# Kernel tuning notes

Measured on AMD Instinct MI355X. Metric: run time of the kernel, lower is better.

## Reference

```python
import jax, jax.numpy as jnp
import numpy as np

B = 8192          # batch_size = len(embedds)
D = 512           # ll_p['num_channels'][-1]
C = 100           # n_classes
N_LAB = 4096      # int(B * plb), plb = 0.5
MAX_ITER = 30     # gtg_i
TOL = 1e-3        # gtg_t
ENT_EPS = 1e-20


def _mlp(x, W1, b1, W2, b2, W3, b3, Wc, bc):
    h = jax.nn.relu(x @ W1 + b1)
    h = jax.nn.relu(h @ W2 + b2)
    h = jax.nn.relu(h @ W3 + b3)
    return (h @ Wc + bc)[:, 0]  # squeeze -> [B]


def _entropy(X):
    # per-row Shannon entropy (bits), as in ALGTG utils
    return -jnp.sum(X * jnp.log2(X + ENT_EPS), axis=1)


def _gtg_entropy_hist(embedds, labels):
    # get_A: cos_sim -> zero diagonal -> clamp [0,1] -> 'mean' threshold -> 'diversity' (1-A)
    n = jnp.maximum(jnp.linalg.norm(embedds, axis=-1, keepdims=True), 1e-12)
    E = embedds / n
    A = E @ E.T                                   # [B,B]
    A = A * (1.0 - jnp.eye(B, dtype=A.dtype))     # fill_diagonal_(0)
    A = jnp.clip(A, 0.0, 1.0)
    A = jnp.where(A < jnp.mean(A), 0.0, A)        # AM_threshold_strategy == 'mean'
    A = 1.0 - A                                   # AM_strategy == 'diversity'

    # get_X: labeled rows one-hot, unlabeled rows uniform 1/C
    lab = jnp.arange(B) < N_LAB
    X0 = jnp.where(lab[:, None],
                   jax.nn.one_hot(labels, C, dtype=jnp.float32),
                   jnp.full((B, C), 1.0 / C, jnp.float32))
    hist0 = jnp.zeros((B, MAX_ITER), jnp.float32)
    unlab = ~lab

    def cond(s):
        _X, _h, i, err = s
        return (err > TOL) & (i < MAX_ITER)

    def body(s):
        X, hist, i, _err = s
        Xn = X * (A @ X)                          # replicator dynamics step
        Xn = Xn / jnp.sum(Xn, axis=1, keepdims=True)
        ent = _entropy(Xn)
        hist = hist.at[:, i].set(jnp.where(unlab, ent, 0.0))
        return (Xn, hist, i + 1, jnp.linalg.norm(Xn - X))

    init = (X0, hist0, jnp.array(0, jnp.int32), jnp.array(jnp.inf, jnp.float32))
    _, hist, _, _ = jax.lax.while_loop(cond, body, init)
    return hist


def setup_inputs() -> dict:
    key = jax.random.key(0)
    ks = jax.random.split(key, 11)
    d2, d4, d8 = D // 2, D // 4, D // 8

    def lin(k, fi, fo):
        return jax.random.normal(k, (fi, fo), jnp.float32) / np.float32(np.sqrt(fi))

    return {
        'features': jax.random.normal(ks[0], (B, 64), jnp.float32),
        'embedds': jax.random.normal(ks[1], (B, D), jnp.float32),
        'labels': jax.random.randint(ks[2], (B,), 0, C),
        'W1': lin(ks[3], D, d2), 'b1': jnp.zeros((d2,), jnp.float32),
        'W2': lin(ks[4], d2, d4), 'b2': jnp.zeros((d4,), jnp.float32),
        'W3': lin(ks[5], d4, d8), 'b3': jnp.zeros((d8,), jnp.float32),
        'Wc': lin(ks[6], d8, 1), 'bc': jnp.zeros((1,), jnp.float32),
    }


def reference(features, embedds, labels, W1, b1, W2, b2, W3, b3, Wc, bc):
    y_pred = _mlp(embedds, W1, b1, W2, b2, W3, b3, Wc, bc)        # [B]
    hist = _gtg_entropy_hist(embedds, labels)                      # [B, MAX_ITER]
    y_true = jnp.mean(hist, axis=1)                                # ent_strategy == 'mean'
    labeled_mask = jnp.arange(B) < N_LAB                           # bool [B]
    return (y_pred, y_true, labeled_mask)
```

## Files before the change

### kernel.cpp

```cpp
#include <hip/hip_runtime.h>
#include <hip/hip_bf16.h>
#include <math.h>

namespace {
constexpr int BROWS = 8192;
constexpr int NLAB  = 4096;
constexpr int NUNL  = 4096;
constexpr int CREAL = 100;
constexpr int CPAD  = 112;
constexpr int DIM   = 512;
constexpr int MAXIT = 30;

constexpr size_t MiB = 1ull << 20;
constexpr size_t OFF_S    = 0;
constexpr size_t OFF_AU   = 64 * MiB;
constexpr size_t OFF_EB   = 96 * MiB;
constexpr size_t OFF_XT0  = 96 * MiB;
constexpr size_t OFF_XT1  = 98 * MiB;
constexpr size_t OFF_XU   = 100 * MiB;
constexpr size_t OFF_PL   = 102 * MiB;
constexpr size_t OFF_HIST = 104 * MiB;
constexpr size_t OFF_ERR  = 104 * MiB + 16384;
constexpr size_t OFF_MS   = 104 * MiB + 16768;
constexpr size_t OFF_RN   = 104 * MiB + 32768;
constexpr size_t MEMSET_LEN = 20480;
}

typedef __attribute__((ext_vector_type(8))) short short8;
typedef __attribute__((ext_vector_type(4))) float floatx4;

__device__ inline ushort f2bf(float f) {
  __hip_bfloat16 h = __float2bfloat16(f);
  union { __hip_bfloat16 b; ushort u; } c; c.b = h; return c.u;
}
__device__ inline float bf2f(ushort u) {
  union { ushort u; __hip_bfloat16 b; } c; c.u = u;
  return __bfloat162float(c.b);
}

__global__ __launch_bounds__(64) void k_prep(const float* __restrict__ emb,
                                             ushort* __restrict__ Eb,
                                             float* __restrict__ rn) {
  int row = blockIdx.x, l = threadIdx.x;
  const float4* e4 = (const float4*)(emb + (size_t)row * DIM);
  float4 a = e4[2 * l], b = e4[2 * l + 1];
  float f[8] = {a.x, a.y, a.z, a.w, b.x, b.y, b.z, b.w};
  float s = 0.f;
#pragma unroll
  for (int q = 0; q < 8; q++) s += f[q] * f[q];
#pragma unroll
  for (int m = 1; m < 64; m <<= 1) s += __shfl_xor(s, m);
  if (l == 0) rn[row] = 1.0f / fmaxf(sqrtf(s), 1e-12f);
  union { short8 v; ushort u[8]; } o;
#pragma unroll
  for (int q = 0; q < 8; q++) o.u[q] = f2bf(f[q]);
  *(short8*)(Eb + (size_t)row * DIM + l * 8) = o.v;
}

__global__ __launch_bounds__(256) void k_initX(ushort* __restrict__ X0,
                                               ushort* __restrict__ X1,
                                               float* __restrict__ Xu,
                                               const int* __restrict__ labels) {
  int j = blockIdx.x * 256 + threadIdx.x;
  int c = blockIdx.y;
  float v;
  if (j < NLAB) v = (labels[j] == c) ? 1.0f : 0.0f;
  else          v = (c < CREAL) ? 0.01f : 0.0f;
  ushort b = f2bf(v);
  X0[(size_t)c * BROWS + j] = b;
  X1[(size_t)c * BROWS + j] = b;
  if (j >= NLAB) Xu[(size_t)(j - NLAB) * CPAD + c] = (c < CREAL) ? 0.01f : 0.0f;
}

__global__ __launch_bounds__(256) void k_mlp(const float* __restrict__ emb,
                                             const float* __restrict__ W1, const float* __restrict__ b1,
                                             const float* __restrict__ W2, const float* __restrict__ b2,
                                             const float* __restrict__ W3, const float* __restrict__ b3,
                                             const float* __restrict__ Wc, const float* __restrict__ bc,
                                             float* __restrict__ out) {
  __shared__ float xs[4][512];
  __shared__ float h1[4][256];
  __shared__ float h2[4][128];
  __shared__ float h3[4][64];
  int t = threadIdx.x;
  int r0 = blockIdx.x * 4;
  {
    const float4* src = (const float4*)(emb + (size_t)r0 * DIM);
    float4* dst = (float4*)&xs[0][0];
    dst[t] = src[t];
    dst[t + 256] = src[t + 256];
  }
  __syncthreads();
  {
    float a0 = 0.f, a1 = 0.f, a2 = 0.f, a3 = 0.f;
    for (int k = 0; k < 512; k++) {
      float w = W1[k * 256 + t];
      a0 = fmaf(xs[0][k], w, a0);
      a1 = fmaf(xs[1][k], w, a1);
      a2 = fmaf(xs[2][k], w, a2);
      a3 = fmaf(xs[3][k], w, a3);
    }
    float bb = b1[t];
    h1[0][t] = fmaxf(a0 + bb, 0.f);
    h1[1][t] = fmaxf(a1 + bb, 0.f);
    h1[2][t] = fmaxf(a2 + bb, 0.f);
    h1[3][t] = fmaxf(a3 + bb, 0.f);
  }
  __syncthreads();
  {
    int c = t & 127, rb = (t >> 7) * 2;
    float a0 = 0.f, a1 = 0.f;
    for (int k = 0; k < 256; k++) {
      float w = W2[k * 128 + c];
      a0 = fmaf(h1[rb][k], w, a0);
      a1 = fmaf(h1[rb + 1][k], w, a1);
    }
    float bb = b2[c];
    h2[rb][c] = fmaxf(a0 + bb, 0.f);
    h2[rb + 1][c] = fmaxf(a1 + bb, 0.f);
  }
  __syncthreads();
  {
    int c = t & 63, r = t >> 6;
    float a = 0.f;
    for (int k = 0; k < 128; k++) a = fmaf(h2[r][k], W3[k * 64 + c], a);
    h3[r][c] = fmaxf(a + b3[c], 0.f);
  }
  __syncthreads();
  {
    int r = t >> 6, l = t & 63;
    float v = h3[r][l] * Wc[l];
#pragma unroll
    for (int m = 32; m; m >>= 1) v += __shfl_down(v, m);
    if (l == 0) out[r0 + r] = v + bc[0];
  }
}

__global__ __launch_bounds__(256) void k_simM(const ushort* __restrict__ Eb,
                                              const float* __restrict__ rn,
                                              ushort* __restrict__ S,
                                              double* __restrict__ meansum) {
  int x = blockIdx.x, y = blockIdx.y;
  if (x < 32 && y > x) return;
  __shared__ ushort Ei[128 * 40];
  __shared__ ushort Ej[128 * 40];
  __shared__ float redbuf[4];

  int t = threadIdx.x;
  int w = t >> 6, lane = t & 63;
  int m = lane & 15, g = lane >> 4;
  int ib = (w >> 1) * 64, jb = (w & 1) * 64;
  int i0 = x * 128, j0 = y * 128;

  floatx4 acc[4][4];
#pragma unroll
  for (int a = 0; a < 4; a++)
#pragma unroll
    for (int b = 0; b < 4; b++) acc[a][b] = (floatx4)0.0f;

  int lrow = t >> 1, lhalf = (t & 1) * 16;
  for (int kt = 0; kt < DIM; kt += 32) {
    __syncthreads();
    {
      const ushort* gi = Eb + (size_t)(i0 + lrow) * DIM + kt + lhalf;
      const ushort* gj = Eb + (size_t)(j0 + lrow) * DIM + kt + lhalf;
      int o = lrow * 40 + lhalf;
      *(short8*)&Ei[o]     = *(const short8*)gi;
      *(short8*)&Ei[o + 8] = *(const short8*)(gi + 8);
      *(short8*)&Ej[o]     = *(const short8*)gj;
      *(short8*)&Ej[o + 8] = *(const short8*)(gj + 8);
    }
    __syncthreads();

    short8 ah[4], bh[4];
#pragma unroll
    for (int rt = 0; rt < 4; rt++) ah[rt] = *(const short8*)&Ei[(ib + rt * 16 + m) * 40 + g * 8];
#pragma unroll
    for (int ct = 0; ct < 4; ct++) bh[ct] = *(const short8*)&Ej[(jb + ct * 16 + m) * 40 + g * 8];
#pragma unroll
    for (int rt = 0; rt < 4; rt++)
#pragma unroll
      for (int ct = 0; ct < 4; ct++)
        acc[rt][ct] = __builtin_amdgcn_mfma_f32_16x16x32_bf16(ah[rt], bh[ct], acc[rt][ct], 0, 0, 0);
  }

  bool dostore = (x >= 32);
  bool isdiag  = (x == y);
  float weight = (x < 32) ? (isdiag ? 1.0f : 2.0f) : ((y < 32) ? 2.0f : 1.0f);
  float lsum = 0.f;
#pragma unroll
  for (int rt = 0; rt < 4; rt++) {
    int gi0 = i0 + ib + rt * 16 + g * 4;
    float4 rni = *(const float4*)(rn + gi0);
#pragma unroll
    for (int ct = 0; ct < 4; ct++) {
      int gj = j0 + jb + ct * 16 + m;
      float rnj = rn[gj];
#pragma unroll
      for (int r = 0; r < 4; r++) {
        int gi = gi0 + r;
        float rv = (r == 0) ? rni.x : (r == 1) ? rni.y : (r == 2) ? rni.z : rni.w;
        float s = acc[rt][ct][r] * rv * rnj;
        if (isdiag && gi == gj) s = 0.f;
        s = fminf(fmaxf(s, 0.f), 1.f);
        lsum += s;
        if (dostore) S[(size_t)(gi - NLAB) * BROWS + gj] = f2bf(s);
      }
    }
  }
  lsum *= weight;
#pragma unroll
  for (int d = 1; d < 64; d <<= 1) lsum += __shfl_xor(lsum, d);
  if (lane == 0) redbuf[w] = lsum;
  __syncthreads();
  if (t == 0) atomicAdd(meansum, (double)(redbuf[0] + redbuf[1] + redbuf[2] + redbuf[3]));
}

__global__ __launch_bounds__(1024, 4) void k_iter(const ushort* __restrict__ S,
                                                  ushort* __restrict__ Au,
                                                  const ushort* __restrict__ XTr,
                                                  ushort* __restrict__ XTw,
                                                  float* __restrict__ Xu,
                                                  float* __restrict__ Plab,
                                                  float* __restrict__ hist,
                                                  float* __restrict__ errsq,
                                                  const double* __restrict__ ms,
                                                  int it) {
  if (it > 0 && errsq[it - 1] <= 1e-6f) return;
  __shared__ float part[8][16 * 113];
  __shared__ float Pbuf[16 * 114];
  __shared__ float dsqbuf[16];
  ushort* xbuf = (ushort*)&part[0][0];
  int t = threadIdx.x;
  int w = t >> 6, lane = t & 63;
  int m = lane & 15, g = lane >> 4;
  int r0 = blockIdx.x * 16;

  float2 xo = make_float2(0.f, 0.f);
  if (lane < 56) xo = *(const float2*)(Xu + (size_t)(r0 + w) * CPAD + lane * 2);
  float pl_pre[2] = {0.f, 0.f};
  if (it > 0) {
#pragma unroll
    for (int q = 0; q < 2; q++) {
      int idx = t + q * 1024;
      if (idx < 16 * CPAD)
        pl_pre[q] = Plab[(size_t)(r0 + idx / CPAD) * CPAD + idx % CPAD];
    }
  }

  floatx4 acc[7];
#pragma unroll
  for (int c = 0; c < 7; c++) acc[c] = (floatx4)0.0f;

  if (it == 0) {
    float mean = (float)(ms[0] * (1.0 / ((double)BROWS * (double)BROWS)));
    int kw = w * 512;
    for (int ks = 0; ks < 16; ks++) {
      int kk = kw + ks * 32;
      size_t so = (size_t)(r0 + m) * BROWS + kk + g * 8;
      short8 a = *(const short8*)(S + so);
      union { short8 v; ushort u[8]; } ua; ua.v = a;
#pragma unroll
      for (int e = 0; e < 8; e++) {
        float s = bf2f(ua.u[e]);
        float av = (s < mean) ? 1.0f : 1.0f - s;
        ua.u[e] = f2bf(av);
      }
      a = ua.v;
      if (w >= 8)
        *(short8*)(Au + (size_t)(r0 + m) * NUNL + (kk - NLAB) + g * 8) = a;
#pragma unroll
      for (int ct = 0; ct < 7; ct++) {
        short8 b = *(const short8*)(XTr + (size_t)(ct * 16 + m) * BROWS + kk + g * 8);
        acc[ct] = __builtin_amdgcn_mfma_f32_16x16x32_bf16(a, b, acc[ct], 0, 0, 0);
      }
    }
  } else {
    int kw = w * 256;
    size_t abase = (size_t)(r0 + m) * NUNL + kw + g * 8;
    size_t bbase = (size_t)m * BROWS + NLAB + kw + g * 8;
    for (int ks = 0; ks < 8; ks++) {
      short8 a = *(const short8*)(Au + abase + ks * 32);
#pragma unroll
      for (int ct = 0; ct < 7; ct++) {
        short8 b = *(const short8*)(XTr + bbase + (size_t)ct * 16 * BROWS + ks * 32);
        acc[ct] = __builtin_amdgcn_mfma_f32_16x16x32_bf16(a, b, acc[ct], 0, 0, 0);
      }
    }
  }

  if (w < 8) {
#pragma unroll
    for (int ct = 0; ct < 7; ct++)
#pragma unroll
      for (int r = 0; r < 4; r++)
        part[w][(g * 4 + r) * 113 + ct * 16 + m] = acc[ct][r];
  }
  __syncthreads();
  float sA[2] = {0.f, 0.f}, sB[2] = {0.f, 0.f};
#pragma unroll
  for (int q = 0; q < 2; q++) {
    int idx = t + q * 1024;
    if (idx < 16 * CPAD) {
      int row = idx / CPAD, col = idx % CPAD;
      int o = row * 113 + col;
      sA[q] = ((part[0][o] + part[1][o]) + (part[2][o] + part[3][o]))
            + ((part[4][o] + part[5][o]) + (part[6][o] + part[7][o]));
    }
  }
  __syncthreads();
  if (w >= 8) {
#pragma unroll
    for (int ct = 0; ct < 7; ct++)
#pragma unroll
      for (int r = 0; r < 4; r++)
        part[w - 8][(g * 4 + r) * 113 + ct * 16 + m] = acc[ct][r];
  }
  __syncthreads();
#pragma unroll
  for (int q = 0; q < 2; q++) {
    int idx = t + q * 1024;
    if (idx < 16 * CPAD) {
      int row = idx / CPAD, col = idx % CPAD;
      int o = row * 113 + col;
      sB[q] = ((part[0][o] + part[1][o]) + (part[2][o] + part[3][o]))
            + ((part[4][o] + part[5][o]) + (part[6][o] + part[7][o]));
      float P;
      size_t go = (size_t)(r0 + row) * CPAD + col;
      if (it == 0) { Plab[go] = sA[q]; P = sA[q] + sB[q]; }
      else         { P = sA[q] + sB[q] + pl_pre[q]; }
      Pbuf[row * 114 + col] = P;
    }
  }
  __syncthreads();

  int gr = r0 + w;
  bool act = lane < 56;
  float2 p = make_float2(0.f, 0.f);
  if (act) p = *(const float2*)&Pbuf[w * 114 + lane * 2];
  float2 xn;
  xn.x = xo.x * p.x;
  xn.y = xo.y * p.y;
  float s = xn.x + xn.y;
#pragma unroll
  for (int d = 1; d < 64; d <<= 1) s += __shfl_xor(s, d);
  float inv = 1.0f / s;
  float ent = 0.f, dsq = 0.f;
  if (act) {
    xn.x *= inv; xn.y *= inv;
    ent = -(xn.x * log2f(xn.x + 1e-20f) + xn.y * log2f(xn.y + 1e-20f));
    float dx = xn.x - xo.x, dy = xn.y - xo.y;
    dsq = dx * dx + dy * dy;
    *(float2*)(Xu + (size_t)gr * CPAD + lane * 2) = xn;
    int c0 = lane * 2;
    xbuf[c0 * 18 + w]       = f2bf(xn.x);
    xbuf[(c0 + 1) * 18 + w] = f2bf(xn.y);
  }
#pragma unroll
  for (int d = 1; d < 64; d <<= 1) { ent += __shfl_xor(ent, d); dsq += __shfl_xor(dsq, d); }
  if (lane == 0) {
    hist[gr] += ent;
    dsqbuf[w] = dsq;
  }
  __syncthreads();

  if (t < CPAD * 8) {
    int c = t >> 3, jl = (t & 7) * 2;
    ushort2 v = *(const ushort2*)&xbuf[c * 18 + jl];
    *(ushort2*)(XTw + (size_t)c * BROWS + NLAB + r0 + jl) = v;
  }
  if (t == 0) {
    float ds = 0.f;
#pragma unroll
    for (int i = 0; i < 16; i++) ds += dsqbuf[i];
    atomicAdd(&errsq[it], ds);
  }
}

__global__ __launch_bounds__(256) void k_final(const float* __restrict__ hist,
                                               float* __restrict__ out) {
  int i = blockIdx.x * 256 + threadIdx.x;
  float yt = (i < NLAB) ? 0.0f : hist[i - NLAB] * (1.0f / 30.0f);
  out[BROWS + i] = yt;
  out[2 * BROWS + i] = (i < NLAB) ? 1.0f : 0.0f;
}

extern "C" void kernel_launch(void* const* d_in, const int* in_sizes, int n_in,
                              void* d_out, int out_size, void* d_ws, size_t ws_size,
                              hipStream_t stream) {
  const float* emb    = (const float*)d_in[1];
  const int*   labels = (const int*)d_in[2];
  const float* W1 = (const float*)d_in[3];
  const float* b1 = (const float*)d_in[4];
  const float* W2 = (const float*)d_in[5];
  const float* b2 = (const float*)d_in[6];
  const float* W3 = (const float*)d_in[7];
  const float* b3 = (const float*)d_in[8];
  const float* Wc = (const float*)d_in[9];
  const float* bc = (const float*)d_in[10];
  float* out = (float*)d_out;

  char* ws = (char*)d_ws;
  ushort* S    = (ushort*)(ws + OFF_S);
  ushort* Au   = (ushort*)(ws + OFF_AU);
  ushort* Eb   = (ushort*)(ws + OFF_EB);
  ushort* XT0  = (ushort*)(ws + OFF_XT0);
  ushort* XT1  = (ushort*)(ws + OFF_XT1);
  float*  Xu   = (float*)(ws + OFF_XU);
  float*  Plab = (float*)(ws + OFF_PL);
  float*  hist = (float*)(ws + OFF_HIST);
  float*  errs = (float*)(ws + OFF_ERR);
  double* ms   = (double*)(ws + OFF_MS);
  float*  rn   = (float*)(ws + OFF_RN);

  hipMemsetAsync(ws + OFF_HIST, 0, MEMSET_LEN, stream);

  k_prep<<<BROWS, 64, 0, stream>>>(emb, Eb, rn);
  k_mlp<<<BROWS / 4, 256, 0, stream>>>(emb, W1, b1, W2, b2, W3, b3, Wc, bc, out);

  { dim3 g(BROWS / 128, BROWS / 128); k_simM<<<g, 256, 0, stream>>>(Eb, rn, S, ms); }

  { dim3 g(BROWS / 256, CPAD); k_initX<<<g, 256, 0, stream>>>(XT0, XT1, Xu, labels); }

  for (int it = 0; it < MAXIT; it++) {
    const ushort* XTr = (it & 1) ? XT1 : XT0;
    ushort*       XTw = (it & 1) ? XT0 : XT1;
    k_iter<<<NUNL / 16, 1024, 0, stream>>>(S, Au, XTr, XTw, Xu, Plab, hist, errs, ms, it);
  }

  k_final<<<BROWS / 256, 256, 0, stream>>>(hist, out);
}
```

Before: 732.2 us.

## Double-buffer similarity GEMM tiles with direct global-to-LDS loads and XOR swizzle

The k_simM similarity GEMM now stages its E tiles with 16-byte global_load_lds instructions, so data goes straight from global memory into shared memory without passing through registers. The shared tiles are double-buffered, and the loads for the next k-step are issued before the MFMAs on the current one, which leaves one barrier per iteration instead of two. The old 40-element padded row stride is replaced by a 32-element stride with an XOR chunk swizzle to avoid LDS bank conflicts. Correctness relies on the barrier waiting for the async loads and on the swizzle matching between the write and read sides.

```diff
diff --git a/kernel.cpp b/kernel.cpp
--- a/kernel.cpp
+++ b/kernel.cpp
@@ -36,6 +36,11 @@
 __device__ inline float bf2f(ushort u) {
   union { ushort u; __hip_bfloat16 b; } c; c.u = u;
   return __bfloat162float(c.b);
+}
+__device__ inline void gl16(const ushort* g, ushort* l) {
+  __builtin_amdgcn_global_load_lds(
+      (const __attribute__((address_space(1))) unsigned int*)g,
+      (__attribute__((address_space(3))) unsigned int*)l, 16, 0, 0);
 }
 
 __global__ __launch_bounds__(64) void k_prep(const float* __restrict__ emb,
@@ -142,8 +147,8 @@
                                               double* __restrict__ meansum) {
   int x = blockIdx.x, y = blockIdx.y;
   if (x < 32 && y > x) return;
-  __shared__ ushort Ei[128 * 40];
-  __shared__ ushort Ej[128 * 40];
+  __shared__ ushort Ei[2][128 * 32];
+  __shared__ ushort Ej[2][128 * 32];
   __shared__ float redbuf[4];
 
   int t = threadIdx.x;
@@ -158,25 +163,34 @@
 #pragma unroll
     for (int b = 0; b < 4; b++) acc[a][b] = (floatx4)0.0f;
 
-  int lrow = t >> 1, lhalf = (t & 1) * 16;
+  int rbase = w * 32;
+  int rl = lane >> 2;
+  int cl = (lane & 3) ^ ((lane >> 3) & 3);
+  int sc = (g ^ ((m >> 1) & 3)) * 8;
+
+#pragma unroll
+  for (int sub = 0; sub < 2; sub++) {
+    int rloc = rbase + sub * 16;
+    gl16(Eb + (size_t)(i0 + rloc + rl) * DIM + cl * 8, &Ei[0][rloc * 32]);
+    gl16(Eb + (size_t)(j0 + rloc + rl) * DIM + cl * 8, &Ej[0][rloc * 32]);
+  }
+
   for (int kt = 0; kt < DIM; kt += 32) {
+    int cur = (kt >> 5) & 1;
     __syncthreads();
-    {
-      const ushort* gi = Eb + (size_t)(i0 + lrow) * DIM + kt + lhalf;
-      const ushort* gj = Eb + (size_t)(j0 + lrow) * DIM + kt + lhalf;
-      int o = lrow * 40 + lhalf;
-      *(short8*)&Ei[o]     = *(const short8*)gi;
-      *(short8*)&Ei[o + 8] = *(const short8*)(gi + 8);
-      *(short8*)&Ej[o]     = *(const short8*)gj;
-      *(short8*)&Ej[o + 8] = *(const short8*)(gj + 8);
-    }
-    __syncthreads();
-
+    if (kt + 32 < DIM) {
+#pragma unroll
+      for (int sub = 0; sub < 2; sub++) {
+        int rloc = rbase + sub * 16;
+        gl16(Eb + (size_t)(i0 + rloc + rl) * DIM + kt + 32 + cl * 8, &Ei[cur ^ 1][rloc * 32]);
+        gl16(Eb + (size_t)(j0 + rloc + rl) * DIM + kt + 32 + cl * 8, &Ej[cur ^ 1][rloc * 32]);
+      }
+    }
     short8 ah[4], bh[4];
 #pragma unroll
-    for (int rt = 0; rt < 4; rt++) ah[rt] = *(const short8*)&Ei[(ib + rt * 16 + m) * 40 + g * 8];
-#pragma unroll
-    for (int ct = 0; ct < 4; ct++) bh[ct] = *(const short8*)&Ej[(jb + ct * 16 + m) * 40 + g * 8];
+    for (int rt = 0; rt < 4; rt++) ah[rt] = *(const short8*)&Ei[cur][(ib + rt * 16 + m) * 32 + sc];
+#pragma unroll
+    for (int ct = 0; ct < 4; ct++) bh[ct] = *(const short8*)&Ej[cur][(jb + ct * 16 + m) * 32 + sc];
 #pragma unroll
     for (int rt = 0; rt < 4; rt++)
 #pragma unroll
```

Result: no change. 743.0 us (+1.5%).
